# Performance work log

Measured on AMD Instinct MI355X. Metric: run time of the kernel, lower is better.

Reference implementation:

```python
import jax, jax.numpy as jnp
import numpy as np

DIM = 1024

def setup_inputs() -> dict:
    key = jax.random.key(0)
    k1, k2, k3, k4, k5 = jax.random.split(key, 5)
    x = jax.random.normal(k1, (4, 2048, DIM), dtype=jnp.float32)
    w_qkv = jax.random.normal(k2, (DIM, 3 * DIM), dtype=jnp.float32) * (DIM ** -0.5)
    b_qkv = jax.random.normal(k3, (3 * DIM,), dtype=jnp.float32) * 0.02
    w_proj = jax.random.normal(k4, (DIM, DIM), dtype=jnp.float32) * (DIM ** -0.5)
    b_proj = jax.random.normal(k5, (DIM,), dtype=jnp.float32) * 0.02
    return {"x": x, "w_qkv": w_qkv, "b_qkv": b_qkv, "w_proj": w_proj, "b_proj": b_proj}

def reference(x, w_qkv, b_qkv, w_proj, b_proj):
    # qkv projection: [B, S, 3*D] -> chunk into q, k, v
    qkv = jnp.einsum('bsd,de->bse', x, w_qkv) + b_qkv
    q, k, v = jnp.split(qkv, 3, axis=-1)
    scale = jnp.asarray(DIM ** 0.5, dtype=x.dtype)  # note: module divides by dim**0.5
    attn = jnp.einsum('bqd,bkd->bqk', q, k) / scale  # [B, S, S]
    attn = jax.nn.softmax(attn, axis=-1)
    out = jnp.einsum('bqk,bkd->bqd', attn, v)
    return jnp.einsum('bsd,de->bse', out, w_proj) + b_proj
```

## Files before the change

kernel.cpp:

```cpp
#include <hip/hip_runtime.h>

typedef unsigned short u16;
typedef __attribute__((ext_vector_type(8))) unsigned short u16x8;
typedef __attribute__((ext_vector_type(8))) short s16x8;
typedef __attribute__((ext_vector_type(4))) float f32x4;

__device__ __forceinline__ u16 f2bf(float f) {
    union { float f; unsigned int u; } c; c.f = f;
    unsigned int u = c.u;
    u += 0x7fffu + ((u >> 16) & 1u);
    return (u16)(u >> 16);
}
__device__ __forceinline__ float bf2f(u16 h) {
    union { unsigned int u; float f; } c; c.u = ((unsigned int)h) << 16; return c.f;
}

__device__ __forceinline__ void gload16(const u16* g, u16* l) {
    __builtin_amdgcn_global_load_lds(
        (const __attribute__((address_space(1))) void*)g,
        (__attribute__((address_space(3))) void*)l, 16, 0, 0);
}

__global__ __launch_bounds__(256) void cast_f32_bf16(const float* __restrict__ in,
                                                     u16* __restrict__ out, int n8) {
    int i = blockIdx.x * 256 + threadIdx.x;
    if (i >= n8) return;
    const float4* p = (const float4*)in;
    float4 a = p[2 * i], b = p[2 * i + 1];
    u16x8 o;
    o[0] = f2bf(a.x); o[1] = f2bf(a.y); o[2] = f2bf(a.z); o[3] = f2bf(a.w);
    o[4] = f2bf(b.x); o[5] = f2bf(b.y); o[6] = f2bf(b.z); o[7] = f2bf(b.w);
    ((u16x8*)out)[i] = o;
}

__global__ __launch_bounds__(256) void transpose_cast_f32(const float* __restrict__ src,
                                                          u16* __restrict__ dst, int R, int C) {
    __shared__ u16 t[32][33];
    int tx = threadIdx.x & 31, ty = threadIdx.x >> 5;
    int c0 = blockIdx.x * 32, r0 = blockIdx.y * 32;
#pragma unroll
    for (int i = 0; i < 4; ++i)
        t[ty + i * 8][tx] = f2bf(src[(size_t)(r0 + ty + i * 8) * C + c0 + tx]);
    __syncthreads();
#pragma unroll
    for (int i = 0; i < 4; ++i)
        dst[(size_t)(c0 + ty + i * 8) * R + r0 + tx] = t[tx][ty + i * 8];
}

__global__ __launch_bounds__(256) void softmax_rows_b16(u16* __restrict__ S) {
    const int t = threadIdx.x;
    u16* row = S + (size_t)blockIdx.x * 2048;
    u16x8 a = ((const u16x8*)row)[t];
    float f[8];
#pragma unroll
    for (int j = 0; j < 8; ++j) f[j] = bf2f(a[j]);
    float m = fmaxf(fmaxf(fmaxf(f[0], f[1]), fmaxf(f[2], f[3])),
                    fmaxf(fmaxf(f[4], f[5]), fmaxf(f[6], f[7])));
#pragma unroll
    for (int o = 32; o >= 1; o >>= 1) m = fmaxf(m, __shfl_xor(m, o));
    __shared__ float sm[4], ss[4];
    if ((t & 63) == 0) sm[t >> 6] = m;
    __syncthreads();
    m = fmaxf(fmaxf(sm[0], sm[1]), fmaxf(sm[2], sm[3]));
    float s = 0.f;
#pragma unroll
    for (int j = 0; j < 8; ++j) { f[j] = __expf(f[j] - m); s += f[j]; }
#pragma unroll
    for (int o = 32; o >= 1; o >>= 1) s += __shfl_xor(s, o);
    if ((t & 63) == 0) ss[t >> 6] = s;
    __syncthreads();
    s = (ss[0] + ss[1]) + (ss[2] + ss[3]);
    float inv = 1.f / s;
    u16x8 o8;
#pragma unroll
    for (int j = 0; j < 8; ++j) o8[j] = f2bf(f[j] * inv);
    ((u16x8*)row)[t] = o8;
}

template<int EPI>
__global__ __launch_bounds__(256, 3) void gemm128(
    const u16* __restrict__ A, const u16* __restrict__ Bt,
    int K, int ldA, int ldBt,
    const float* __restrict__ bias,
    float* __restrict__ outF, int ldOutF,
    u16* __restrict__ outH, int ldOutH,
    u16* __restrict__ Qo, u16* __restrict__ Ko, u16* __restrict__ Vo,
    size_t zA, size_t zBt, size_t zOut) {
    __shared__ u16 lds[16384];
    const int tid  = threadIdx.x;
    const int lane = tid & 63;
    const int wave = tid >> 6;
    const int wrow = wave >> 1, wcol = wave & 1;
    const int lrow = lane & 15;
    const int lkg  = lane >> 4;
    const int bm0  = blockIdx.x * 128;
    const int bn0  = blockIdx.y * 128;
    A  += zA  * blockIdx.z;
    Bt += zBt * blockIdx.z;

    const int srow = tid >> 3;
    const int ssc  = (((tid & 7) * 16) ^ ((srow & 7) << 4)) >> 1;
    const u16* aS[4];
    const u16* bS[4];
#pragma unroll
    for (int g = 0; g < 4; ++g) {
        aS[g] = A  + (size_t)(bm0 + g * 32 + srow) * ldA  + ssc;
        bS[g] = Bt + (size_t)(bn0 + g * 32 + srow) * ldBt + ssc;
    }
    const int dst = wave * 512;

    const int sc0 = (lkg * 16) ^ ((lrow & 7) << 4);
    const int sc1 = (64 + lkg * 16) ^ ((lrow & 7) << 4);

    f32x4 acc[4][4] = {};
    const int NT = K >> 6;

    for (int t = 0; t < NT; ++t) {
#pragma unroll
        for (int g = 0; g < 4; ++g) {
            gload16(aS[g] + (size_t)t * 64, lds + g * 2048 + dst);
            gload16(bS[g] + (size_t)t * 64, lds + 8192 + g * 2048 + dst);
        }
        __syncthreads();
        const char* base = (const char*)lds;
        s16x8 ra[4][2], rb[4][2];
#pragma unroll
        for (int i = 0; i < 4; ++i) {
            const char* p = base + (wrow * 64 + i * 16 + lrow) * 128;
            ra[i][0] = *(const s16x8*)(p + sc0);
            ra[i][1] = *(const s16x8*)(p + sc1);
        }
#pragma unroll
        for (int j = 0; j < 4; ++j) {
            const char* p = base + 16384 + (wcol * 64 + j * 16 + lrow) * 128;
            rb[j][0] = *(const s16x8*)(p + sc0);
            rb[j][1] = *(const s16x8*)(p + sc1);
        }
#pragma unroll
        for (int ks = 0; ks < 2; ++ks)
#pragma unroll
            for (int i = 0; i < 4; ++i)
#pragma unroll
                for (int j = 0; j < 4; ++j)
                    acc[i][j] = __builtin_amdgcn_mfma_f32_16x16x32_bf16(
                        ra[i][ks], rb[j][ks], acc[i][j], 0, 0, 0);
        __syncthreads();
    }

    if constexpr (EPI == 1) outF += zOut * blockIdx.z;
    else if constexpr (EPI == 2 || EPI == 4) outH += zOut * blockIdx.z;
#pragma unroll
    for (int i = 0; i < 4; ++i) {
        int row0 = bm0 + wrow * 64 + i * 16 + lkg * 4;
#pragma unroll
        for (int j = 0; j < 4; ++j) {
            int col = bn0 + wcol * 64 + j * 16 + lrow;
#pragma unroll
            for (int r = 0; r < 4; ++r) {
                int row = row0 + r;
                float v = acc[i][j][r];
                if constexpr (EPI == 0) {
                    v += bias[col];
                    if (col < 1024)       Qo[(size_t)row * 1024 + col] = f2bf(v * 0.03125f);
                    else if (col < 2048)  Ko[(size_t)row * 1024 + (col - 1024)] = f2bf(v);
                    else                  Vo[(size_t)row * 1024 + (col - 2048)] = f2bf(v);
                } else if constexpr (EPI == 1) {
                    outF[(size_t)row * ldOutF + col] = v;
                } else if constexpr (EPI == 2) {
                    outH[(size_t)row * ldOutH + col] = f2bf(v);
                } else {
                    outH[(size_t)row * ldOutH + col] = f2bf(v + bias[row]);
                }
            }
        }
    }
}

extern "C" void kernel_launch(void* const* d_in, const int* in_sizes, int n_in,
                              void* d_out, int out_size, void* d_ws, size_t ws_size,
                              hipStream_t stream) {
    const float* x      = (const float*)d_in[0];
    const float* w_qkv  = (const float*)d_in[1];
    const float* b_qkv  = (const float*)d_in[2];
    const float* w_proj = (const float*)d_in[3];
    const float* b_proj = (const float*)d_in[4];
    float* out = (float*)d_out;
    char* ws = (char*)d_ws;
    (void)in_sizes; (void)n_in; (void)out_size;

    const size_t MB16  = 16777216;
    const size_t BATCH = 2097152;
    const size_t SZB   = 4194304;
    const size_t VPB   = 2097152;

    if (ws_size >= 85983232) {
        u16* xb     = (u16*)(ws);
        u16* Qb     = (u16*)(ws + MB16);
        u16* Kb     = (u16*)(ws + 2 * MB16);
        u16* Vb     = (u16*)(ws + 3 * MB16);
        u16* wqkvT  = (u16*)(ws + 4 * MB16);
        u16* wprojT = (u16*)(ws + 4 * MB16 + 6291456);
        u16* Vpt    = xb;
        u16* Sb     = Vb;

        cast_f32_bf16<<<4096, 256, 0, stream>>>(x, xb, 1048576);
        transpose_cast_f32<<<dim3(96, 32), 256, 0, stream>>>(w_qkv, wqkvT, 1024, 3072);
        transpose_cast_f32<<<dim3(32, 32), 256, 0, stream>>>(w_proj, wprojT, 1024, 1024);
        gemm128<0><<<dim3(64, 24), 256, 0, stream>>>(xb, wqkvT, 1024, 1024, 1024,
                                                     b_qkv, nullptr, 0, nullptr, 0,
                                                     Qb, Kb, Vb, 0, 0, 0);
        gemm128<4><<<dim3(8, 16, 4), 256, 0, stream>>>(wprojT, Vb, 1024, 1024, 1024,
                                                       b_proj, nullptr, 0, Vpt, 2048,
                                                       nullptr, nullptr, nullptr,
                                                       0, BATCH, VPB);
        gemm128<2><<<dim3(16, 16, 4), 256, 0, stream>>>(Qb, Kb, 1024, 1024, 1024,
                                                        nullptr, nullptr, 0, Sb, 2048,
                                                        nullptr, nullptr, nullptr,
                                                        BATCH, BATCH, SZB);
        softmax_rows_b16<<<8192, 256, 0, stream>>>(Sb);
        gemm128<1><<<dim3(16, 8, 4), 256, 0, stream>>>(Sb, Vpt, 2048, 2048, 2048,
                                                       nullptr, out, 1024, nullptr, 0,
                                                       nullptr, nullptr, nullptr,
                                                       SZB, VPB, BATCH);
    } else {
        u16* xbB    = (u16*)(ws);
        u16* QbB    = (u16*)(ws + 4194304);
        u16* KbB    = (u16*)(ws + 8388608);
        u16* VbB    = (u16*)(ws + 12582912);
        u16* VptB   = (u16*)(ws + 16777216);
        u16* Sb     = (u16*)(ws + 20971520);
        u16* wqkvT  = (u16*)(ws + 29360128);
        u16* wprojT = (u16*)(ws + 35651584);

        transpose_cast_f32<<<dim3(96, 32), 256, 0, stream>>>(w_qkv, wqkvT, 1024, 3072);
        transpose_cast_f32<<<dim3(32, 32), 256, 0, stream>>>(w_proj, wprojT, 1024, 1024);
        for (int b = 0; b < 4; ++b) {
            cast_f32_bf16<<<1024, 256, 0, stream>>>(x + (size_t)b * BATCH, xbB, 262144);
            gemm128<0><<<dim3(16, 24), 256, 0, stream>>>(xbB, wqkvT, 1024, 1024, 1024,
                                                         b_qkv, nullptr, 0, nullptr, 0,
                                                         QbB, KbB, VbB, 0, 0, 0);
            gemm128<4><<<dim3(8, 16), 256, 0, stream>>>(wprojT, VbB, 1024, 1024, 1024,
                                                        b_proj, nullptr, 0, VptB, 2048,
                                                        nullptr, nullptr, nullptr, 0, 0, 0);
            gemm128<2><<<dim3(16, 16), 256, 0, stream>>>(QbB, KbB, 1024, 1024, 1024,
                                                         nullptr, nullptr, 0, Sb, 2048,
                                                         nullptr, nullptr, nullptr, 0, 0, 0);
            softmax_rows_b16<<<2048, 256, 0, stream>>>(Sb);
            gemm128<1><<<dim3(16, 8), 256, 0, stream>>>(Sb, VptB, 2048, 2048, 2048,
                                                        nullptr, out + (size_t)b * BATCH, 1024,
                                                        nullptr, 0,
                                                        nullptr, nullptr, nullptr, 0, 0, 0);
        }
    }
}
```

Baseline: 202.1 us.

## Add 256x256 ping-pong pipelined GEMM for QKV projection and QK^T

Adds a new 512-thread GEMM kernel with 256x256 output tiles that double-buffers LDS loads through direct global-to-LDS transfers. It interleaves the staged loads with four MFMA quadrants per K-step, using barriers and s_setprio to let the two waves per SIMD alternate. The kernel is used for the QKV projection and for the Q·K^T score GEMM in place of the 128x128 kernel, aiming for more reuse per loaded byte and better overlap of memory and matrix work. In exchange it uses 128KB of LDS per block and many registers, and launches fewer blocks.

```diff
diff --git a/kernel.cpp b/kernel.cpp
--- a/kernel.cpp
+++ b/kernel.cpp
@@ -176,6 +176,151 @@
     }
 }
 
+template<int MB, int NB>
+__device__ __forceinline__ void mfma_quad(f32x4 (&acc)[8][4], const s16x8 (&ra)[4][2],
+                                          const s16x8 (&rb)[2][2]) {
+    __builtin_amdgcn_s_setprio(1);
+#pragma unroll
+    for (int ks = 0; ks < 2; ++ks)
+#pragma unroll
+        for (int i = 0; i < 4; ++i)
+#pragma unroll
+            for (int j = 0; j < 2; ++j)
+                acc[MB + i][NB + j] = __builtin_amdgcn_mfma_f32_16x16x32_bf16(
+                    ra[i][ks], rb[j][ks], acc[MB + i][NB + j], 0, 0, 0);
+    __builtin_amdgcn_s_setprio(0);
+}
+
+template<int EPI>
+__global__ __launch_bounds__(512, 2) void gemm256p(
+    const u16* __restrict__ A, const u16* __restrict__ Bt,
+    int K, int ldA, int ldBt,
+    const float* __restrict__ bias,
+    u16* __restrict__ outH, int ldOutH,
+    u16* __restrict__ Qo, u16* __restrict__ Ko, u16* __restrict__ Vo,
+    size_t zA, size_t zBt, size_t zOut) {
+    __shared__ u16 lds[65536];
+    const int tid  = threadIdx.x;
+    const int lane = tid & 63;
+    const int wave = tid >> 6;
+    const int wm   = wave >> 2;
+    const int wn   = wave & 3;
+    const int lrow = lane & 15;
+    const int lkg  = lane >> 4;
+    const int bm0  = blockIdx.x * 256;
+    const int bn0  = blockIdx.y * 256;
+    A  += zA  * blockIdx.z;
+    Bt += zBt * blockIdx.z;
+
+    const int NT = K >> 6;
+
+    const int srow = tid >> 3;
+    const int ssc  = (((tid & 7) * 16) ^ ((srow & 7) << 4)) >> 1;
+    const u16* aBase = A  + (size_t)(bm0 + srow) * ldA  + ssc;
+    const u16* bBase = Bt + (size_t)(bn0 + srow) * ldBt + ssc;
+    const int dwave  = wave * 512;
+    const int slotBase[4] = {16384, 24576, 0, 8192};
+
+#define STAGEH(h)                                                                  \
+    if ((h) < 4 * NT) {                                                            \
+        const int j_ = (h) >> 2, q_ = (h) & 3, hf_ = q_ & 1;                       \
+        const u16* s_ = (q_ & 2) ? aBase : bBase;                                  \
+        const int ld_ = (q_ & 2) ? ldA : ldBt;                                     \
+        u16* d_ = lds + (j_ & 1) * 32768 + slotBase[q_] + dwave;                   \
+        gload16(s_ + (size_t)(hf_ * 128) * ld_ + j_ * 64, d_);                     \
+        gload16(s_ + (size_t)(hf_ * 128 + 64) * ld_ + j_ * 64, d_ + 4096);         \
+    }
+
+    const char* ldsc = (const char*)lds;
+    const int sc0 = (lkg * 16) ^ ((lrow & 7) << 4);
+    const int sc1 = (64 + lkg * 16) ^ ((lrow & 7) << 4);
+    const int aOff = wm * 16384;
+    const int bOff = 32768 + (wn >> 1) * 16384;
+    const int brow = (wn & 1) * 64;
+
+    f32x4 acc[8][4] = {};
+    s16x8 regA[4][2], regB0[2][2], regB1[2][2];
+
+    STAGEH(0) STAGEH(1) STAGEH(2) STAGEH(3) STAGEH(4) STAGEH(5) STAGEH(6)
+    asm volatile("s_waitcnt vmcnt(6)" ::: "memory");
+    __builtin_amdgcn_s_barrier();
+
+    for (int j = 0; j < NT; ++j) {
+        const char* bA = ldsc + (j & 1) * 65536 + aOff;
+        const char* bB = ldsc + (j & 1) * 65536 + bOff;
+        const int h0 = 4 * j + 7;
+#pragma unroll
+        for (int i = 0; i < 4; ++i) {
+            const char* p = bA + (i * 16 + lrow) * 128;
+            regA[i][0] = *(const s16x8*)(p + sc0);
+            regA[i][1] = *(const s16x8*)(p + sc1);
+        }
+#pragma unroll
+        for (int jf = 0; jf < 2; ++jf) {
+            const char* p = bB + (brow + jf * 16 + lrow) * 128;
+            regB0[jf][0] = *(const s16x8*)(p + sc0);
+            regB0[jf][1] = *(const s16x8*)(p + sc1);
+        }
+        STAGEH(h0)
+        __builtin_amdgcn_s_barrier();
+        mfma_quad<0, 0>(acc, regA, regB0);
+        __builtin_amdgcn_s_barrier();
+#pragma unroll
+        for (int jf = 0; jf < 2; ++jf) {
+            const char* p = bB + (brow + 32 + jf * 16 + lrow) * 128;
+            regB1[jf][0] = *(const s16x8*)(p + sc0);
+            regB1[jf][1] = *(const s16x8*)(p + sc1);
+        }
+        STAGEH(h0 + 1)
+        __builtin_amdgcn_s_barrier();
+        mfma_quad<0, 2>(acc, regA, regB1);
+        __builtin_amdgcn_s_barrier();
+#pragma unroll
+        for (int i = 0; i < 4; ++i) {
+            const char* p = bA + (64 + i * 16 + lrow) * 128;
+            regA[i][0] = *(const s16x8*)(p + sc0);
+            regA[i][1] = *(const s16x8*)(p + sc1);
+        }
+        STAGEH(h0 + 2)
+        __builtin_amdgcn_s_barrier();
+        mfma_quad<4, 2>(acc, regA, regB1);
+        __builtin_amdgcn_s_barrier();
+        STAGEH(h0 + 3)
+        if (j < NT - 3) {
+            asm volatile("s_waitcnt vmcnt(6)" ::: "memory");
+        } else {
+            asm volatile("s_waitcnt vmcnt(0)" ::: "memory");
+        }
+        __builtin_amdgcn_s_barrier();
+        mfma_quad<4, 0>(acc, regA, regB0);
+        __builtin_amdgcn_s_barrier();
+    }
+#undef STAGEH
+
+    if constexpr (EPI == 2) outH += zOut * blockIdx.z;
+#pragma unroll
+    for (int mf = 0; mf < 8; ++mf) {
+        int row0 = bm0 + wm * 128 + mf * 16 + lkg * 4;
+#pragma unroll
+        for (int nf = 0; nf < 4; ++nf) {
+            int col = bn0 + wn * 64 + nf * 16 + lrow;
+#pragma unroll
+            for (int r = 0; r < 4; ++r) {
+                int row = row0 + r;
+                float v = acc[mf][nf][r];
+                if constexpr (EPI == 0) {
+                    v += bias[col];
+                    if (col < 1024)       Qo[(size_t)row * 1024 + col] = f2bf(v * 0.03125f);
+                    else if (col < 2048)  Ko[(size_t)row * 1024 + (col - 1024)] = f2bf(v);
+                    else                  Vo[(size_t)row * 1024 + (col - 2048)] = f2bf(v);
+                } else {
+                    outH[(size_t)row * ldOutH + col] = f2bf(v);
+                }
+            }
+        }
+    }
+}
+
 extern "C" void kernel_launch(void* const* d_in, const int* in_sizes, int n_in,
                               void* d_out, int out_size, void* d_ws, size_t ws_size,
                               hipStream_t stream) {
@@ -206,17 +351,17 @@
         cast_f32_bf16<<<4096, 256, 0, stream>>>(x, xb, 1048576);
         transpose_cast_f32<<<dim3(96, 32), 256, 0, stream>>>(w_qkv, wqkvT, 1024, 3072);
         transpose_cast_f32<<<dim3(32, 32), 256, 0, stream>>>(w_proj, wprojT, 1024, 1024);
-        gemm128<0><<<dim3(64, 24), 256, 0, stream>>>(xb, wqkvT, 1024, 1024, 1024,
-                                                     b_qkv, nullptr, 0, nullptr, 0,
-                                                     Qb, Kb, Vb, 0, 0, 0);
+        gemm256p<0><<<dim3(32, 12), 512, 0, stream>>>(xb, wqkvT, 1024, 1024, 1024,
+                                                      b_qkv, nullptr, 0,
+                                                      Qb, Kb, Vb, 0, 0, 0);
         gemm128<4><<<dim3(8, 16, 4), 256, 0, stream>>>(wprojT, Vb, 1024, 1024, 1024,
                                                        b_proj, nullptr, 0, Vpt, 2048,
                                                        nullptr, nullptr, nullptr,
                                                        0, BATCH, VPB);
-        gemm128<2><<<dim3(16, 16, 4), 256, 0, stream>>>(Qb, Kb, 1024, 1024, 1024,
-                                                        nullptr, nullptr, 0, Sb, 2048,
-                                                        nullptr, nullptr, nullptr,
-                                                        BATCH, BATCH, SZB);
+        gemm256p<2><<<dim3(8, 8, 4), 512, 0, stream>>>(Qb, Kb, 1024, 1024, 1024,
+                                                       nullptr, Sb, 2048,
+                                                       nullptr, nullptr, nullptr,
+                                                       BATCH, BATCH, SZB);
         softmax_rows_b16<<<8192, 256, 0, stream>>>(Sb);
         gemm128<1><<<dim3(16, 8, 4), 256, 0, stream>>>(Sb, Vpt, 2048, 2048, 2048,
                                                        nullptr, out, 1024, nullptr, 0,
```

After: 208.9 us. 3.3% more time.
